# Performance work log

Measured on AMD Instinct MI355X. Metric: run time of the kernel, lower is better.

Reference implementation:

```python
import jax, jax.numpy as jnp
import numpy as np

B, S, D_IN, D_MODEL = 128, 2048, 512, 2048
M, NSY, H, T = 25, 64, 8, 10
REP = NSY * (NSY + 1) // 2
OUT_DIMS = S * 2
DH = D_IN // H
IU, JU = np.triu_indices(NSY)
IDX_OUT = np.arange(NSY)                      # 'first-last': first n neurons for out sync
IDX_ACT = np.arange(D_MODEL - NSY, D_MODEL)   # last n neurons for action sync


def _ln(x, g, b):
    mu = x.mean(-1, keepdims=True)
    var = x.var(-1, keepdims=True)
    return (x - mu) / jnp.sqrt(var + 1e-5) * g + b


def _sync(act, alpha, beta, r, idx):
    # pairwise upper-triangle outer product without materializing (B,n,n)
    sel = act[:, idx]
    pair = sel[:, IU] * sel[:, JU]  # (B, REP)
    if alpha is None:
        alpha, beta = pair, jnp.ones_like(pair)
    else:
        alpha = r * alpha + pair
        beta = r * beta + 1.0
    return alpha / jnp.sqrt(beta), alpha, beta


def _forward(tokens, emb, W_pos, b_pos, Wq, bq, Wk, bk, Wv, bv, Wo, bo, Ws, bs,
             ln_s_g, ln_s_b, ln_n_g, ln_n_b, Wn, bn, temp, Wout, bout,
             start_act, start_trace, decay_action, decay_out):
    # rotary-style learned positional embedding: rotate [0,1] by theta in [0,180deg]
    thetas = jnp.deg2rad(jnp.linspace(0.0, 180.0, S))
    rotated = jnp.stack([-jnp.sin(thetas), jnp.cos(thetas)], -1)  # (S,2)
    pe = rotated @ W_pos + b_pos                                   # (S, D_IN)
    feats = emb[tokens] + pe[None]                                 # (B,S,D_IN)
    kh = (feats @ Wk + bk).reshape(B, S, H, DH)
    vh = (feats @ Wv + bv).reshape(B, S, H, DH)
    r_a = jnp.exp(-decay_action)[None]
    r_o = jnp.exp(-decay_out)[None]
    act = jnp.broadcast_to(start_act[None], (B, D_MODEL))
    trace = jnp.broadcast_to(start_trace[None], (B, D_MODEL, M))
    a_a = b_a = a_o = b_o = None
    preds, certs = [], []
    for _ in range(T):
        s_act, a_a, b_a = _sync(act, a_a, b_a, r_a, IDX_ACT)
        q = (s_act @ Wq + bq).reshape(B, H, DH)
        scores = jnp.einsum('bhd,bshd->bhs', q, kh) / np.float32(np.sqrt(DH))
        attn = jax.nn.softmax(scores, -1)
        o = jnp.einsum('bhs,bshd->bhd', attn, vh).reshape(B, D_IN) @ Wo + bo
        # SynapseNet: Linear -> GLU -> LayerNorm
        pre = jnp.concatenate([o, act], -1) @ Ws + bs
        g1, g2 = jnp.split(pre, 2, -1)
        state = _ln(g1 * jax.nn.sigmoid(g2), ln_s_g, ln_s_b)  # (B, D_MODEL)
        trace = jnp.concatenate([trace[:, :, 1:], state[:, :, None]], -1)
        # NLM: per-neuron linear over memory, GLU, temperature
        xn = _ln(trace, ln_n_g, ln_n_b)
        y = jnp.einsum('bnm,mon->bno', xn, Wn) + bn  # (B, D_MODEL, 2)
        act = (y[..., 0] * jax.nn.sigmoid(y[..., 1])) / temp
        s_out, a_o, b_o = _sync(act, a_o, b_o, r_o, IDX_OUT)
        pred = s_out @ Wout + bout  # (B, OUT_DIMS)
        preds.append(pred)
        logits = pred.reshape(B, S, 2)
        p = jax.nn.softmax(logits, -1)
        ent = -(p * jax.nn.log_softmax(logits, -1)).sum(-1) / np.float32(np.log(2.0))
        ne = ent.mean(-1)
        certs.append(jnp.stack([ne, 1.0 - ne], -1))
    return jnp.stack(preds, -1), jnp.stack(certs, -1)  # (B,OUT_DIMS,T),(B,2,T)


def setup_inputs() -> dict:
    key = jax.random.key(0)
    ks = jax.random.split(key, 16)
    def n(k, shape, s=0.02):
        return (jax.random.normal(k, shape) * s).astype(jnp.float32)
    bound = 1.0 / np.sqrt(M + 2)
    return {
        'tokens': jax.random.randint(ks[0], (B, S), 0, 2, dtype=jnp.int32),
        'emb': n(ks[1], (2, D_IN), 1.0),
        'W_pos': n(ks[2], (2, D_IN)), 'b_pos': jnp.zeros((D_IN,)),
        'Wq': n(ks[3], (REP, D_IN)), 'bq': jnp.zeros((D_IN,)),
        'Wk': n(ks[4], (D_IN, D_IN)), 'bk': jnp.zeros((D_IN,)),
        'Wv': n(ks[5], (D_IN, D_IN)), 'bv': jnp.zeros((D_IN,)),
        'Wo': n(ks[6], (D_IN, D_IN)), 'bo': jnp.zeros((D_IN,)),
        'Ws': n(ks[7], (D_IN + D_MODEL, 2 * D_MODEL)), 'bs': jnp.zeros((2 * D_MODEL,)),
        'ln_s_g': jnp.ones((D_MODEL,)), 'ln_s_b': jnp.zeros((D_MODEL,)),
        'ln_n_g': jnp.ones((M,)), 'ln_n_b': jnp.zeros((M,)),
        'Wn': jax.random.uniform(ks[8], (M, 2, D_MODEL), minval=-bound, maxval=bound),
        'bn': jnp.zeros((1, D_MODEL, 2)),
        'temp': jnp.ones((1,)),
        'Wout': n(ks[9], (REP, OUT_DIMS)), 'bout': jnp.zeros((OUT_DIMS,)),
        'start_act': n(ks[10], (D_MODEL,), 1.0),
        'start_trace': n(ks[11], (D_MODEL, M), 1.0),
        'decay_action': jax.random.uniform(ks[12], (REP,), minval=0.0, maxval=1.0),
        'decay_out': jax.random.uniform(ks[13], (REP,), minval=0.0, maxval=1.0),
    }


def reference(tokens, emb, W_pos, b_pos, Wq, bq, Wk, bk, Wv, bv, Wo, bo, Ws, bs,
              ln_s_g, ln_s_b, ln_n_g, ln_n_b, Wn, bn, temp, Wout, bout,
              start_act, start_trace, decay_action, decay_out):
    return _forward(tokens, emb, W_pos, b_pos, Wq, bq, Wk, bk, Wv, bv, Wo, bo, Ws, bs,
                    ln_s_g, ln_s_b, ln_n_g, ln_n_b, Wn, bn, temp, Wout, bout,
                    start_act, start_trace, decay_action, decay_out)
```

## Files before the change

### kernel.cpp

```cpp
#include <hip/hip_runtime.h>
#include <hip/hip_bf16.h>
#include <math.h>

#define B_ 128
#define S_ 2048
#define D_IN_ 512
#define D_MODEL_ 2048
#define M_ 25
#define NSY_ 64
#define H_ 8
#define T_ 10
#define REP_ 2080
#define DH_ 64
#define PRED_N (B_ * 4096)

typedef unsigned short ushort_t;
typedef __bf16 bf16x8 __attribute__((ext_vector_type(8)));
typedef float f32x4 __attribute__((ext_vector_type(4)));
typedef unsigned short us8 __attribute__((ext_vector_type(8)));

__device__ __forceinline__ ushort_t f2bf(float f) {
    __hip_bfloat16 h = __float2bfloat16(f);
    return *(ushort_t*)&h;
}
// ... 90 lines not shown
    const ushort_t* __restrict__ A, int lda,
    const ushort_t* __restrict__ Bt, int ldb,
    const float* __restrict__ bias,
    float* __restrict__ C, int ldc,
    int M, int N, int K, int kchunk)
{
    const int nb = blockIdx.x, mb = blockIdx.y, zb = blockIdx.z;
    const int k0 = zb * kchunk;
    const int k1 = min(K, k0 + kchunk);
    __shared__ ushort_t As[64][40];
    __shared__ ushort_t Bs[128][40];

    const int tid  = threadIdx.x;
    const int wave = tid >> 6;
    const int lane = tid & 63;
    const int quad = lane >> 4;
    const int mrow = lane & 15;

    f32x4 acc[4][2];
    #pragma unroll
    for (int s = 0; s < 4; s++)
        #pragma unroll
        for (int u = 0; u < 2; u++)
            acc[s][u] = (f32x4){0.f, 0.f, 0.f, 0.f};

    const int arow = tid >> 2, akc = (tid & 3) * 8;
    const int brow = tid >> 1, bkc = (tid & 1) * 16;

    for (int kk0 = k0; kk0 < k1; kk0 += 32) {
        {
            const ushort_t* ap = A + (size_t)(mb * 64 + arow) * lda + kk0 + akc;
            *(us8*)&As[arow][akc] = *(const us8*)ap;
        }
        {
            const ushort_t* bp = Bt + (size_t)(nb * 128 + brow) * ldb + kk0 + bkc;
            *(us8*)&Bs[brow][bkc]     = *(const us8*)bp;
            *(us8*)&Bs[brow][bkc + 8] = *(const us8*)(bp + 8);
        }
        __syncthreads();

        bf16x8 af[4], bfr[2];
        #pragma unroll
        for (int s = 0; s < 4; s++)
            af[s] = *(const bf16x8*)&As[s * 16 + mrow][quad * 8];
        #pragma unroll
        for (int u = 0; u < 2; u++)
            bfr[u] = *(const bf16x8*)&Bs[wave * 32 + u * 16 + mrow][quad * 8];
        #pragma unroll
        for (int s = 0; s < 4; s++)
            #pragma unroll
            for (int u = 0; u < 2; u++)
                acc[s][u] = __builtin_amdgcn_mfma_f32_16x16x32_bf16(
                    af[s], bfr[u], acc[s][u], 0, 0, 0);
        __syncthreads();
    }

    if (gridDim.z == 1) {
        #pragma unroll
        for (int s = 0; s < 4; s++)
            #pragma unroll
            for (int u = 0; u < 2; u++) {
                const int col = nb * 128 + wave * 32 + u * 16 + mrow;
                #pragma unroll
                for (int reg = 0; reg < 4; reg++) {
                    const int row = mb * 64 + s * 16 + quad * 4 + reg;
                    C[(size_t)row * ldc + col] = acc[s][u][reg] + bias[col];
                }
            }
    } else {
        #pragma unroll
        for (int s = 0; s < 4; s++)
            #pragma unroll
            for (int u = 0; u < 2; u++) {
                const int col = nb * 128 + wave * 32 + u * 16 + mrow;
                #pragma unroll
                for (int reg = 0; reg < 4; reg++) {
                    const int row = mb * 64 + s * 16 + quad * 4 + reg;
                    atomicAdd(&C[(size_t)row * ldc + col], acc[s][u][reg]);
                }
            }
    }
}

__global__ __launch_bounds__(256) void gemm_bb_dual(
    const ushort_t* __restrict__ A1, int lda1,
    const ushort_t* __restrict__ Bt1, int ldb1,
    float* __restrict__ C1, int ldc1, int kc1, int nb1x, int nblk1,
    const ushort_t* __restrict__ A2, int lda2,
    const ushort_t* __restrict__ Bt2, int ldb2,
    float* __restrict__ C2, int ldc2, int kc2, int nb2x)
{
    int bid = blockIdx.x;
    const ushort_t* A; const ushort_t* Bt; float* C;
    int lda, ldb, ldc, nb, mb, zb, kchunk;
    if (bid < nblk1) {
        A = A1; Bt = Bt1; C = C1; lda = lda1; ldb = ldb1; ldc = ldc1; kchunk = kc1;
        nb = bid % nb1x; mb = (bid / nb1x) & 1; zb = bid / (nb1x * 2);
    } else {
        bid -= nblk1;
        A = A2; Bt = Bt2; C = C2; lda = lda2; ldb = ldb2; ldc = ldc2; kchunk = kc2;
        nb = bid % nb2x; mb = (bid / nb2x) & 1; zb = bid / (nb2x * 2);
    }
    const int k0 = zb * kchunk;
    const int k1 = min(REP_, k0 + kchunk);
    __shared__ ushort_t As[64][40];
    __shared__ ushort_t Bs[128][40];

    const int tid  = threadIdx.x;
    const int wave = tid >> 6;
    const int lane = tid & 63;
    const int quad = lane >> 4;
    const int mrow = lane & 15;

    f32x4 acc[4][2];
    #pragma unroll
    for (int s = 0; s < 4; s++)
        #pragma unroll
        for (int u = 0; u < 2; u++)
            acc[s][u] = (f32x4){0.f, 0.f, 0.f, 0.f};

    const int arow = tid >> 2, akc = (tid & 3) * 8;
    const int brow = tid >> 1, bkc = (tid & 1) * 16;

    for (int kk0 = k0; kk0 < k1; kk0 += 32) {
        {
            const ushort_t* ap = A + (size_t)(mb * 64 + arow) * lda + kk0 + akc;
            *(us8*)&As[arow][akc] = *(const us8*)ap;
        }
        {
            const ushort_t* bp = Bt + (size_t)(nb * 128 + brow) * ldb + kk0 + bkc;
            *(us8*)&Bs[brow][bkc]     = *(const us8*)bp;
            *(us8*)&Bs[brow][bkc + 8] = *(const us8*)(bp + 8);
        }
        __syncthreads();

        bf16x8 af[4], bfr[2];
        #pragma unroll
        for (int s = 0; s < 4; s++)
            af[s] = *(const bf16x8*)&As[s * 16 + mrow][quad * 8];
        #pragma unroll
        for (int u = 0; u < 2; u++)
            bfr[u] = *(const bf16x8*)&Bs[wave * 32 + u * 16 + mrow][quad * 8];
        #pragma unroll
        for (int s = 0; s < 4; s++)
            #pragma unroll
            for (int u = 0; u < 2; u++)
                acc[s][u] = __builtin_amdgcn_mfma_f32_16x16x32_bf16(
                    af[s], bfr[u], acc[s][u], 0, 0, 0);
        __syncthreads();
    }

    #pragma unroll
    for (int s = 0; s < 4; s++)
        #pragma unroll
        for (int u = 0; u < 2; u++) {
            const int col = nb * 128 + wave * 32 + u * 16 + mrow;
            #pragma unroll
            for (int reg = 0; reg < 4; reg++) {
                const int row = mb * 64 + s * 16 + quad * 4 + reg;
                atomicAdd(&C[(size_t)row * ldc + col], acc[s][u][reg]);
            }
        }
}

__global__ __launch_bounds__(256) void gemm_qk(
    const float* __restrict__ q,
    const ushort_t* __restrict__ Kb,
    float* __restrict__ sc)
{
    const int nb = blockIdx.x, mb = blockIdx.y, z = blockIdx.z;
    const int c = z >> 3, h = z & 7;
    __shared__ ushort_t As[64][40];
    __shared__ ushort_t Bs[128][40];

    const int tid  = threadIdx.x;
    const int wave = tid >> 6;
    const int lane = tid & 63;
    const int quad = lane >> 4;
    const int mrow = lane & 15;

    f32x4 acc[4][2];
    #pragma unroll
    for (int s = 0; s < 4; s++)
        #pragma unroll
        for (int u = 0; u < 2; u++)
            acc[s][u] = (f32x4){0.f, 0.f, 0.f, 0.f};

    const int arow = tid >> 2, akc = (tid & 3) * 8;
    const int brow = tid >> 1, bkc = (tid & 1) * 16;
    const float* Abase = q + (size_t)h * 64;
    const ushort_t* Bbase = Kb + (size_t)c * S_ * 512 + h * 64;

    #pragma unroll
    for (int kk0 = 0; kk0 < 64; kk0 += 32) {
        {
            const float* ap = Abase + (size_t)(mb * 64 + arow) * 512 + kk0 + akc;
            float4 v0 = *(const float4*)ap;
            float4 v1 = *(const float4*)(ap + 4);
            us8 w = { f2bf(v0.x), f2bf(v0.y), f2bf(v0.z), f2bf(v0.w),
                      f2bf(v1.x), f2bf(v1.y), f2bf(v1.z), f2bf(v1.w) };
            *(us8*)&As[arow][akc] = w;
        }
        {
            const ushort_t* bp = Bbase + (size_t)(nb * 128 + brow) * 512 + kk0 + bkc;
            *(us8*)&Bs[brow][bkc]     = *(const us8*)bp;
            *(us8*)&Bs[brow][bkc + 8] = *(const us8*)(bp + 8);
        }
        __syncthreads();

        bf16x8 af[4], bfr[2];
        #pragma unroll
        for (int s = 0; s < 4; s++)
            af[s] = *(const bf16x8*)&As[s * 16 + mrow][quad * 8];
        #pragma unroll
        for (int u = 0; u < 2; u++)
            bfr[u] = *(const bf16x8*)&Bs[wave * 32 + u * 16 + mrow][quad * 8];
        #pragma unroll
        for (int s = 0; s < 4; s++)
            #pragma unroll
            for (int u = 0; u < 2; u++)
                acc[s][u] = __builtin_amdgcn_mfma_f32_16x16x32_bf16(
                    af[s], bfr[u], acc[s][u], 0, 0, 0);
        __syncthreads();
    }

    float* Cb = sc + (size_t)z * 128 * S_;
    #pragma unroll
    for (int s = 0; s < 4; s++)
        #pragma unroll
        for (int u = 0; u < 2; u++) {
            const int col = nb * 128 + wave * 32 + u * 16 + mrow;
            #pragma unroll
            for (int reg = 0; reg < 4; reg++) {
                const int row = mb * 64 + s * 16 + quad * 4 + reg;
                Cb[(size_t)row * S_ + col] = 0.125f * acc[s][u][reg];
            }
        }
}

__global__ __launch_bounds__(256) void attn_soft(
    const float* __restrict__ sc,
    const int*   __restrict__ tokens,
    ushort_t* __restrict__ P,
    float* __restrict__ o,
    float* __restrict__ cat,
    const float* __restrict__ bo,
    const float* __restrict__ bs,
    float* __restrict__ pre)
{
    const int bh = blockIdx.x;
    const int b = bh >> 3, h = bh & 7;
    __shared__ float red[256];
    const int tid = threadIdx.x;

    if (bh < 256) {
        const int idx = bh * 256 + tid;
        cat[(size_t)(idx >> 9) * 2560 + (idx & 511)] = bo[idx & 511];
    } else if (bh < 320) {
        const int idx = (bh - 256) * 256 + tid;
        *(float4*)&o[idx * 4] = make_float4(0.f, 0.f, 0.f, 0.f);
    } else if (bh < 832) {
        const int idx = (bh - 320) * 256 + tid;
        const float4* bs4 = (const float4*)bs;
        ((float4*)pre)[idx] = bs4[idx & 1023];
    }

    const float* sc0 = sc + ((size_t)h * 128 + b) * S_;
    const float* sc1 = sc + ((size_t)(8 + h) * 128 + b) * S_;
    const int* trow = tokens + (size_t)b * S_;

    int tok[8]; float sel[8];
    float lmax = -1e30f;
    #pragma unroll
    for (int i = 0; i < 8; i++) {
        const int s = tid + i * 256;
        tok[i] = trow[s];
        sel[i] = tok[i] ? sc1[s] : sc0[s];
        lmax = fmaxf(lmax, sel[i]);
    }
    red[tid] = lmax; __syncthreads();
    for (int off = 128; off > 0; off >>= 1) {
        if (tid < off) red[tid] = fmaxf(red[tid], red[tid + off]);
        __syncthreads();
    }
    const float mx = red[0];
    __syncthreads();

    float e[8];
    float lsum = 0.f;
    #pragma unroll
    for (int i = 0; i < 8; i++) {
        e[i] = expf(sel[i] - mx);
        lsum += e[i];
    }
    red[tid] = lsum; __syncthreads();
    for (int off = 128; off > 0; off >>= 1) {
        if (tid < off) red[tid] += red[tid + off];
        __syncthreads();
    }
    const float inv = 1.f / red[0];

    ushort_t* Pb = P + ((size_t)h * 128 + b) * 4096;
    #pragma unroll
    for (int i = 0; i < 8; i++) {
        const int s = tid + i * 256;
        const unsigned p = (unsigned)f2bf(e[i] * inv);
        const unsigned word = tok[i] ? (p << 16) : p;
        *(unsigned*)&Pb[s * 2] = word;
    }
}

__global__ __launch_bounds__(256) void gemm_pv(
    const ushort_t* __restrict__ P,
    const ushort_t* __restrict__ VT,
    float* __restrict__ o)
{
    const int mb = blockIdx.x, h = blockIdx.y, zb = blockIdx.z;
    const int k0 = zb * 512;
    __shared__ ushort_t As[64][40];
    __shared__ ushort_t Bs[64][40];

    const int tid  = threadIdx.x;
    const int wave = tid >> 6;
    const int lane = tid & 63;
    const int quad = lane >> 4;
    const int mrow = lane & 15;

    f32x4 acc[4];
    #pragma unroll
    for (int s = 0; s < 4; s++) acc[s] = (f32x4){0.f, 0.f, 0.f, 0.f};

    const int row = tid >> 2, kc = (tid & 3) * 8;
    const ushort_t* Ab = P  + ((size_t)h * 128 + mb * 64 + row) * 4096;
    const ushort_t* Bb = VT + ((size_t)h * 64 + row) * 4096;

    for (int kk = k0; kk < k0 + 512; kk += 32) {
        *(us8*)&As[row][kc] = *(const us8*)(Ab + kk + kc);
        *(us8*)&Bs[row][kc] = *(const us8*)(Bb + kk + kc);
        __syncthreads();
        bf16x8 bfr = *(const bf16x8*)&Bs[wave * 16 + mrow][quad * 8];
        #pragma unroll
        for (int s = 0; s < 4; s++) {
            bf16x8 af = *(const bf16x8*)&As[s * 16 + mrow][quad * 8];
            acc[s] = __builtin_amdgcn_mfma_f32_16x16x32_bf16(af, bfr, acc[s], 0, 0, 0);
        }
        __syncthreads();
    }

    const int col = h * 64 + wave * 16 + mrow;
    #pragma unroll
    for (int s = 0; s < 4; s++)
        #pragma unroll
        for (int reg = 0; reg < 4; reg++) {
            const int rowi = mb * 64 + s * 16 + quad * 4 + reg;
            atomicAdd(&o[(size_t)rowi * 512 + col], acc[s][reg]);
        }
}

__global__ void build_vt(const float* __restrict__ Vtab, ushort_t* __restrict__ VT)
{
    const int gid = blockIdx.x * 256 + threadIdx.x;
    const int k = gid & 4095;
    const int d = (gid >> 12) & 63;
    const int h = gid >> 18;
    const int s = k >> 1, c = k & 1;
    VT[gid] = f2bf(Vtab[((size_t)(c * S_ + s)) * 512 + h * 64 + d]);
}

__global__ void build_sync_tabs(const float* __restrict__ dec_act,
                                const float* __restrict__ dec_out,
                                int* __restrict__ ijtab,
                                float* __restrict__ r_act,
                                float* __restrict__ r_out,
                                float* __restrict__ sqb_act,
                                float* __restrict__ sqb_out)
{
    const int p = blockIdx.x * 256 + threadIdx.x;
    if (p >= REP_) return;
    int i = 0, rem = p;
    while (rem >= NSY_ - i) { rem -= NSY_ - i; i++; }
    ijtab[p] = (i << 16) | (i + rem);
    const float ra = expf(-dec_act[p]);
    const float ro = expf(-dec_out[p]);
    r_act[p] = ra; r_out[p] = ro;
    float ba = 1.f, bo2 = 1.f;
    sqb_act[p] = 1.f;
    sqb_out[p] = 1.f;
    for (int t = 1; t < T_; t++) {
        ba  = ra * ba  + 1.f;
        bo2 = ro * bo2 + 1.f;
        sqb_act[(size_t)t * REP_ + p] = sqrtf(ba);
        sqb_out[(size_t)t * REP_ + p] = sqrtf(bo2);
    }
}

__global__ __launch_bounds__(256) void transpose_bf16_kernel(
    const float* __restrict__ in, ushort_t* __restrict__ out, int K, int N)
{
    __shared__ float tile[32][33];
    const int k0 = blockIdx.y * 32, n0 = blockIdx.x * 32;
    const int tx = threadIdx.x & 31, ty4 = (threadIdx.x >> 5) * 4;
    #pragma unroll
    for (int i = 0; i < 4; i++)
        tile[ty4 + i][tx] = in[(size_t)(k0 + ty4 + i) * N + n0 + tx];
    __syncthreads();
    #pragma unroll
    for (int i = 0; i < 4; i++)
        out[(size_t)(n0 + ty4 + i) * K + k0 + tx] = f2bf(tile[tx][ty4 + i]);
}

__global__ void cast_bf16_kernel(const float* __restrict__ src,
                                 __hip_bfloat16* __restrict__ dst, int n)
{
    const int gid = (blockIdx.x * 256 + threadIdx.x) * 4;
    if (gid >= n) return;
    float4 v = *(const float4*)(src + gid);
    dst[gid + 0] = __float2bfloat16(v.x);
    dst[gid + 1] = __float2bfloat16(v.y);
    dst[gid + 2] = __float2bfloat16(v.z);
    dst[gid + 3] = __float2bfloat16(v.w);
}

__global__ void feats_kernel(const float* __restrict__ emb,
                             const float* __restrict__ Wp,
                             const float* __restrict__ bp,
                             float* __restrict__ f2)
{
    const int gid = blockIdx.x * 256 + threadIdx.x;
    const int k = gid & 511;
    const int s = (gid >> 9) & (S_ - 1);
    const int c = gid >> 20;
    const float th = 3.14159265358979323846f * (float)s / (float)(S_ - 1);
    f2[gid] = emb[c * 512 + k] + (-sinf(th)) * Wp[k] + cosf(th) * Wp[512 + k] + bp[k];
}

__global__ void init_act_kernel(const float* __restrict__ sa,
                                float* __restrict__ act,
                                float* __restrict__ cat)
{
    const int gid = blockIdx.x * 256 + threadIdx.x;
    const int b = gid >> 11, n = gid & 2047;
    const float v = sa[n];
    act[gid] = v;
    cat[(size_t)b * 2560 + 512 + n] = v;
}

__global__ void init_trace_kernel(const float* __restrict__ st,
                                  float* __restrict__ trace)
{
    const int gid = blockIdx.x * 256 + threadIdx.x;
    trace[gid] = st[gid % (D_MODEL_ * M_)];
}

__global__ void sync_kernel(const float* __restrict__ act,
                            float* __restrict__ alpha,
                            const float* __restrict__ decay,
                            const int t, const int off,
                            ushort_t* __restrict__ sout,
                            float* __restrict__ ib1, const float* __restrict__ bias1, int iN1,
                            float* __restrict__ ib2, const float* __restrict__ bias2, int iN2)
{
    const int b = blockIdx.x;
    const int tid = threadIdx.x;
    if (blockIdx.y == 8) {
        if (ib1)
            for (int n = tid; n < iN1; n += 256)
                ib1[(size_t)b * iN1 + n] = bias1[n];
        if (ib2)
            for (int n = tid; n < iN2; n += 256)
                ib2[(size_t)b * iN2 + n] = bias2[n];
    }
    const int p = blockIdx.y * 256 + tid;
    if (p >= REP_) return;
    int i = 0, rem = p;
    while (rem >= NSY_ - i) { rem -= NSY_ - i; i++; }
    const int j = i + rem;
    const float si = act[(size_t)b * D_MODEL_ + off + i];
    const float sj = act[(size_t)b * D_MODEL_ + off + j];
    const float pair = si * sj;
    const float r = expf(-decay[p]);
    float a;
    if (t == 0) a = pair;
    else        a = r * alpha[(size_t)b * REP_ + p] + pair;
    alpha[(size_t)b * REP_ + p] = a;
    float bta = 1.f;
    for (int k = 0; k < t; k++) bta = r * bta + 1.f;
    sout[(size_t)b * REP_ + p] = f2bf(a / sqrtf(bta));
}

__global__ __launch_bounds__(512, 2) void state_trace_kernel(
    const float* __restrict__ pre,
    const float* __restrict__ g,
    const float* __restrict__ bt,
    float* __restrict__ trace,
    const float* __restrict__ ln_g,
    const float* __restrict__ ln_b,
    const float* __restrict__ Wn,
    const float* __restrict__ bn,
    const float* __restrict__ temp,
    float* __restrict__ act,
    float* __restrict__ cat,
    const int t,
    const int* __restrict__ ijtab,
    const float* __restrict__ r_out,
    const float* __restrict__ sqb_out,
    float* __restrict__ a_o,
    ushort_t* __restrict__ s_outb,
    const float* __restrict__ bout,
    float* __restrict__ predt,
    const float* __restrict__ r_act,
    const float* __restrict__ sqb_act,
    float* __restrict__ a_a,
    ushort_t* __restrict__ s_actb,
    const float* __restrict__ bq,
    float* __restrict__ qbuf,
    const int do_act)
{
    const int b = blockIdx.x >> 1, half = blockIdx.x & 1;
    const int tid = threadIdx.x;
    __shared__ float v[D_MODEL_];
    __shared__ float r1[512], r2[512];
    __shared__ float sh_sync[64];
    float s1 = 0.f, s2 = 0.f;
    #pragma unroll
    for (int i = 0; i < 4; i++) {
        const int dd = tid + i * 512;
        const float g1 = pre[(size_t)b * 4096 + dd];
        const float g2 = pre[(size_t)b * 4096 + 2048 + dd];
        const float val = g1 * (1.f / (1.f + expf(-g2)));
        v[dd] = val; s1 += val; s2 += val * val;
    }
    r1[tid] = s1; r2[tid] = s2; __syncthreads();
    for (int off = 256; off > 0; off >>= 1) {
        if (tid < off) { r1[tid] += r1[tid + off]; r2[tid] += r2[tid + off]; }
        __syncthreads();
    }
    const float mu = r1[0] * (1.f / D_MODEL_);
    const float var = fmaxf(r2[0] * (1.f / D_MODEL_) - mu * mu, 0.f);
    const float sinv = 1.f / sqrtf(var + 1e-5f);
    const float tval = temp[0];

    #pragma unroll
    for (int i = 0; i < 2; i++) {
        const int n = half * 1024 + i * 512 + tid;
        const float sval = (v[n] - mu) * sinv * g[n] + bt[n];
        const int gid = b * 2048 + n;
        float* tr = trace + (size_t)gid * M_;
        float x[M_];
        #pragma unroll
        for (int m = 0; m < M_ - 1; m++) x[m] = tr[m + 1];
        x[M_ - 1] = sval;
        #pragma unroll
        for (int m = 0; m < M_; m++) tr[m] = x[m];
        float t1 = 0.f, t2 = 0.f;
        #pragma unroll
        for (int m = 0; m < M_; m++) { t1 += x[m]; t2 += x[m] * x[m]; }
        const float tmu = t1 * (1.f / M_);
        const float tvar = fmaxf(t2 * (1.f / M_) - tmu * tmu, 0.f);
        const float tinv = 1.f / sqrtf(tvar + 1e-5f);
        float y0 = bn[n * 2 + 0], y1 = bn[n * 2 + 1];
        #pragma unroll
        for (int m = 0; m < M_; m++) {
            const float xn = (x[m] - tmu) * tinv * ln_g[m] + ln_b[m];
            y0 += xn * Wn[(size_t)(m * 2 + 0) * D_MODEL_ + n];
            y1 += xn * Wn[(size_t)(m * 2 + 1) * D_MODEL_ + n];
        }
        const float a = y0 * (1.f / (1.f + expf(-y1))) / tval;
        act[gid] = a;
        cat[(size_t)b * 2560 + 512 + n] = a;
        if (half == 0) {
            if (i == 0 && tid < 64) sh_sync[tid] = a;
        } else {
            if (i == 1 && tid >= 448) sh_sync[tid - 448] = a;
        }
    }
    __syncthreads();

    if (half == 0) {
        for (int p = tid; p < REP_; p += 512) {
            const int ij = ijtab[p];
            const float pair = sh_sync[ij >> 16] * sh_sync[ij & 0xffff];
            const float r = r_out[p];
            float a2;
            if (t == 0) a2 = pair;
            else        a2 = r * a_o[(size_t)b * REP_ + p] + pair;
            a_o[(size_t)b * REP_ + p] = a2;
            s_outb[(size_t)b * REP_ + p] = f2bf(a2 / sqb_out[(size_t)t * REP_ + p]);
        }
        const float4* b4 = (const float4*)bout;
        float4* pd = (float4*)(predt + (size_t)b * 4096);
        for (int idx = tid; idx < 1024; idx += 512) pd[idx] = b4[idx];
    } else if (do_act) {
        for (int p = tid; p < REP_; p += 512) {
            const int ij = ijtab[p];
            const float pair = sh_sync[ij >> 16] * sh_sync[ij & 0xffff];
            const float r = r_act[p];
            float a2 = r * a_a[(size_t)b * REP_ + p] + pair;
            a_a[(size_t)b * REP_ + p] = a2;
            s_actb[(size_t)b * REP_ + p] = f2bf(a2 / sqb_act[(size_t)(t + 1) * REP_ + p]);
        }
        const float4* b4 = (const float4*)bq;
        float4* qb = (float4*)(qbuf + (size_t)b * 512);
        if (tid < 128) qb[tid] = b4[tid];
    }
}

__global__ __launch_bounds__(256) void ent_all_kernel(
    const float* __restrict__ predst,
    float* __restrict__ certbf)
{
    const int t = blockIdx.x >> 7;
    const int b = blockIdx.x & 127;
    const int tid = threadIdx.x;
    __shared__ float red[256];
    const float* pr = predst + (size_t)t * PRED_N + (size_t)b * 4096;
    float sum = 0.f;
    #pragma unroll
    for (int i = 0; i < 8; i++) {
        const int s = tid + i * 256;
        const float l0 = pr[2 * s], l1 = pr[2 * s + 1];
        const float mm = fmaxf(l0, l1);
        const float z0 = expf(l0 - mm), z1 = expf(l1 - mm);
        const float Z = z0 + z1;
        const float lz = logf(Z);
        const float p0 = z0 / Z, p1 = z1 / Z;
        const float lp0 = (l0 - mm) - lz, lp1 = (l1 - mm) - lz;
        sum += -(p0 * lp0 + p1 * lp1) * 1.4426950408889634f;
    }
    red[tid] = sum; __syncthreads();
    for (int off = 128; off > 0; off >>= 1) {
        if (tid < off) red[tid] += red[tid + off];
        __syncthreads();
    }
    if (tid == 0) {
        const float ne = red[0] * (1.f / S_);
        certbf[(size_t)t * B_ * 2 + b * 2 + 0] = ne;
        certbf[(size_t)t * B_ * 2 + b * 2 + 1] = 1.f - ne;
    }
}

__global__ __launch_bounds__(256) void finalize_kernel(
    const float* __restrict__ predstage,
    const float* __restrict__ certbuf,
    float* __restrict__ dout)
{
    __shared__ float tile[T_][1024];
    const int tid = threadIdx.x;
    const int row0 = blockIdx.x * 1024;
    #pragma unroll
    for (int t = 0; t < T_; t++) {
        float4 v = *(const float4*)(predstage + (size_t)t * PRED_N + row0 + tid * 4);
        tile[t][tid * 4 + 0] = v.x; tile[t][tid * 4 + 1] = v.y;
        tile[t][tid * 4 + 2] = v.z; tile[t][tid * 4 + 3] = v.w;
    }
    __syncthreads();
    float buf[40];
    #pragma unroll
    for (int r = 0; r < 4; r++)
        #pragma unroll
        for (int t = 0; t < T_; t++)
            buf[r * 10 + t] = tile[t][tid * 4 + r];
    float* dst = dout + (size_t)(row0 + tid * 4) * T_;
    #pragma unroll
    for (int k = 0; k < 10; k++)
        *(float4*)(dst + k * 4) = make_float4(buf[4*k], buf[4*k+1], buf[4*k+2], buf[4*k+3]);

    if (blockIdx.x == 0 && tid < B_) {
        const int b = tid;
        const size_t base = (size_t)PRED_N * T_;
        #pragma unroll
        for (int t = 0; t < T_; t++) {
            dout[base + (size_t)(b * 2 + 0) * T_ + t] = certbuf[t * B_ * 2 + b * 2 + 0];
            dout[base + (size_t)(b * 2 + 1) * T_ + t] = certbuf[t * B_ * 2 + b * 2 + 1];
        }
    }
}

extern "C" void kernel_launch(void* const* d_in, const int* in_sizes, int n_in,
                              void* d_out, int out_size, void* d_ws, size_t ws_size,
                              hipStream_t stream)
{
    const int*   tokens    = (const int*)  d_in[0];
    const float* emb       = (const float*)d_in[1];
    const float* W_pos     = (const float*)d_in[2];
    const float* b_pos     = (const float*)d_in[3];
    const float* Wq        = (const float*)d_in[4];
    const float* bq        = (const float*)d_in[5];
    const float* Wk        = (const float*)d_in[6];
    const float* bk        = (const float*)d_in[7];
    const float* Wv        = (const float*)d_in[8];
    const float* bv        = (const float*)d_in[9];
    const float* Wo        = (const float*)d_in[10];
    const float* bo        = (const float*)d_in[11];
    const float* Ws        = (const float*)d_in[12];
    const float* bs        = (const float*)d_in[13];
    const float* ln_s_g    = (const float*)d_in[14];
    const float* ln_s_b    = (const float*)d_in[15];
    const float* ln_n_g    = (const float*)d_in[16];
    const float* ln_n_b    = (const float*)d_in[17];
    const float* Wn        = (const float*)d_in[18];
    const float* bn        = (const float*)d_in[19];
    const float* temp      = (const float*)d_in[20];
    const float* Wout      = (const float*)d_in[21];
    const float* bout      = (const float*)d_in[22];
    const float* start_act = (const float*)d_in[23];
    const float* start_tr  = (const float*)d_in[24];
    const float* dec_act   = (const float*)d_in[25];
    const float* dec_out   = (const float*)d_in[26];
    float* out = (float*)d_out;
    float* w = (float*)d_ws;

    size_t off = 0;
    float* f2     = w + off; off += (size_t)2 * S_ * 512;
    float* Ktab   = w + off; off += (size_t)2 * S_ * 512;
    float* Vtab   = w + off; off += (size_t)2 * S_ * 512;
    float* act    = w + off; off += (size_t)B_ * D_MODEL_;
    float* cat    = w + off; off += (size_t)B_ * 2560;
    float* a_a    = w + off; off += (size_t)B_ * REP_;
    float* a_o    = w + off; off += (size_t)B_ * REP_;
    float* qbuf   = w + off; off += (size_t)B_ * 512;
    float* o_attn = w + off; off += (size_t)B_ * 512;
    float* pre    = w + off; off += (size_t)B_ * 4096;
    float* trace  = w + off; off += (size_t)B_ * D_MODEL_ * M_;
    float* scbuf  = w + off; off += (size_t)16 * 128 * S_;
    float* predst = w + off; off += (size_t)T_ * PRED_N;
    float* certbf = w + off; off += (size_t)T_ * B_ * 2;
    ushort_t* s_actb = (ushort_t*)(w + off); off += (size_t)B_ * REP_ / 2;
    ushort_t* s_outb = (ushort_t*)(w + off); off += (size_t)B_ * REP_ / 2;
    __hip_bfloat16* Kb = (__hip_bfloat16*)(w + off); off += (size_t)S_ * 512;
    ushort_t* Pbuf  = (ushort_t*)(w + off); off += (size_t)8 * 128 * 4096 / 2;
    ushort_t* VT    = (ushort_t*)(w + off); off += (size_t)8 * 64 * 4096 / 2;
    ushort_t* WkT   = (ushort_t*)(w + off); off += (size_t)512 * 512 / 2;
    ushort_t* WvT   = (ushort_t*)(w + off); off += (size_t)512 * 512 / 2;
    ushort_t* WqT   = (ushort_t*)(w + off); off += (size_t)512 * REP_ / 2;
    ushort_t* WoT   = (ushort_t*)(w + off); off += (size_t)512 * 512 / 2;
    ushort_t* WsT   = (ushort_t*)(w + off); off += (size_t)4096 * 2560 / 2;
    ushort_t* WoutT = (ushort_t*)(w + off); off += (size_t)4096 * REP_ / 2;
    int*   ijtab = (int*)(w + off); off += REP_;
    float* r_actT = w + off; off += REP_;
    float* r_outT = w + off; off += REP_;
    float* sqb_a  = w + off; off += (size_t)T_ * REP_;
    float* sqb_o  = w + off; off += (size_t)T_ * REP_;

    feats_kernel<<<(2 * S_ * 512) / 256, 256, 0, stream>>>(emb, W_pos, b_pos, f2);
    init_act_kernel<<<(B_ * D_MODEL_) / 256, 256, 0, stream>>>(start_act, act, cat);
    init_trace_kernel<<<(B_ * D_MODEL_ * M_) / 256, 256, 0, stream>>>(start_tr, trace);
    build_sync_tabs<<<(REP_ + 255) / 256, 256, 0, stream>>>(
        dec_act, dec_out, ijtab, r_actT, r_outT, sqb_a, sqb_o);

    transpose_bf16_kernel<<<dim3(512 / 32, 512 / 32), 256, 0, stream>>>(Wk, WkT, 512, 512);
    transpose_bf16_kernel<<<dim3(512 / 32, 512 / 32), 256, 0, stream>>>(Wv, WvT, 512, 512);
    transpose_bf16_kernel<<<dim3(512 / 32, REP_ / 32), 256, 0, stream>>>(Wq, WqT, REP_, 512);
    transpose_bf16_kernel<<<dim3(512 / 32, 512 / 32), 256, 0, stream>>>(Wo, WoT, 512, 512);
    transpose_bf16_kernel<<<dim3(4096 / 32, 2560 / 32), 256, 0, stream>>>(Ws, WsT, 2560, 4096);
    transpose_bf16_kernel<<<dim3(4096 / 32, REP_ / 32), 256, 0, stream>>>(Wout, WoutT, REP_, 4096);

    gemm_bf16<<<dim3(512 / 128, (2 * S_) / 64, 1), 256, 0, stream>>>(
        f2, 512, WkT, 512, bk, Ktab, 512, 2 * S_, 512, 512, 512);
    gemm_bf16<<<dim3(512 / 128, (2 * S_) / 64, 1), 256, 0, stream>>>(
        f2, 512, WvT, 512, bv, Vtab, 512, 2 * S_, 512, 512, 512);
    cast_bf16_kernel<<<(2 * S_ * 512 / 4) / 256, 256, 0, stream>>>(Ktab, Kb, 2 * S_ * 512);
    build_vt<<<(8 * 64 * 4096) / 256, 256, 0, stream>>>(Vtab, VT);

    sync_kernel<<<dim3(B_, 9), 256, 0, stream>>>(
        act, a_a, dec_act, 0, D_MODEL_ - NSY_, s_actb,
        qbuf, bq, 512, nullptr, nullptr, 0);
    gemm_bb<<<dim3(512 / 128, 2, 13), 256, 0, stream>>>(
        s_actb, REP_, WqT, REP_, bq, qbuf, 512, B_, 512, REP_, 160);

    for (int t = 0; t < T_; t++) {
        gemm_qk<<<dim3(S_ / 128, 2, 16), 256, 0, stream>>>(
            qbuf, (const ushort_t*)Kb, scbuf);
        attn_soft<<<B_ * H_, 256, 0, stream>>>(
            scbuf, tokens, Pbuf, o_attn, cat, bo, bs, pre);
        gemm_pv<<<dim3(2, 8, 8), 256, 0, stream>>>(Pbuf, VT, o_attn);

        gemm_bf16<<<dim3(512 / 128, 2, 8), 256, 0, stream>>>(
            o_attn, 512, WoT, 512, bo, cat, 2560, B_, 512, 512, 64);

        gemm_bf16<<<dim3(4096 / 128, 2, 8), 256, 0, stream>>>(
            cat, 2560, WsT, 2560, bs, pre, 4096, B_, 4096, 2560, 320);

        float* predt = predst + (size_t)t * PRED_N;
        state_trace_kernel<<<B_ * 2, 512, 0, stream>>>(
            pre, ln_s_g, ln_s_b, trace, ln_n_g, ln_n_b, Wn, bn, temp, act, cat,
            t, ijtab,
            r_outT, sqb_o, a_o, s_outb, bout, predt,
            r_actT, sqb_a, a_a, s_actb, bq, qbuf, (t < T_ - 1) ? 1 : 0);

        const int blocks2 = (t < T_ - 1) ? 104 : 0;
        gemm_bb_dual<<<dim3(320 + blocks2), 256, 0, stream>>>(
            s_outb, REP_, WoutT, REP_, predt, 4096, 416, 32, 320,
            s_actb, REP_, WqT, REP_, qbuf, 512, 160, 4);
    }

    ent_all_kernel<<<T_ * B_, 256, 0, stream>>>(predst, certbf);
    finalize_kernel<<<PRED_N / 1024, 256, 0, stream>>>(predst, certbf, out);
}
```

Measured before the change: 1.216 ms.

## Fold Wo into Ws, split the synapse GEMM, and turn the trace into a ring buffer

Precomputes a combined Wo·Ws weight and bias so the attention output goes straight into the synapse pre-activation, removing the per-step Wo GEMM and the concat buffer. The activation half of the synapse GEMM for the next step is computed inside a merged triple kernel, together with the out-sync and action-sync GEMMs, using double-buffered pre arrays. The trace update becomes a ring buffer indexed by a compile-time step, writing one slot instead of shifting all 25. Init and transpose kernels are also merged into single launches. In exchange it adds a one-time weight-combination GEMM and changes the rounding path, since the Wo·Ws product is rounded to bf16.

```diff
diff --git a/kernel.cpp b/kernel.cpp
--- a/kernel.cpp
+++ b/kernel.cpp
@@ -196,31 +196,12 @@
     }
 }
 
-__global__ __launch_bounds__(256) void gemm_bb_dual(
-    const ushort_t* __restrict__ A1, int lda1,
-    const ushort_t* __restrict__ Bt1, int ldb1,
-    float* __restrict__ C1, int ldc1, int kc1, int nb1x, int nblk1,
-    const ushort_t* __restrict__ A2, int lda2,
-    const ushort_t* __restrict__ Bt2, int ldb2,
-    float* __restrict__ C2, int ldc2, int kc2, int nb2x)
-{
-    int bid = blockIdx.x;
-    const ushort_t* A; const ushort_t* Bt; float* C;
-    int lda, ldb, ldc, nb, mb, zb, kchunk;
-    if (bid < nblk1) {
-        A = A1; Bt = Bt1; C = C1; lda = lda1; ldb = ldb1; ldc = ldc1; kchunk = kc1;
-        nb = bid % nb1x; mb = (bid / nb1x) & 1; zb = bid / (nb1x * 2);
-    } else {
-        bid -= nblk1;
-        A = A2; Bt = Bt2; C = C2; lda = lda2; ldb = ldb2; ldc = ldc2; kchunk = kc2;
-        nb = bid % nb2x; mb = (bid / nb2x) & 1; zb = bid / (nb2x * 2);
-    }
-    const int k0 = zb * kchunk;
-    const int k1 = min(REP_, k0 + kchunk);
-    __shared__ ushort_t As[64][40];
-    __shared__ ushort_t Bs[128][40];
-
-    const int tid  = threadIdx.x;
+__device__ __forceinline__ void g_tile128(
+    const ushort_t* Ap, int lda, const ushort_t* Bt, int ldb,
+    float* C, int ldc, int nb, int mb, int k0, int k1, char* smem, int tid)
+{
+    ushort_t (*As)[40] = (ushort_t(*)[40])smem;
+    ushort_t (*Bs)[40] = (ushort_t(*)[40])(smem + 64 * 40 * 2);
     const int wave = tid >> 6;
     const int lane = tid & 63;
     const int quad = lane >> 4;
@@ -238,7 +219,7 @@
 
     for (int kk0 = k0; kk0 < k1; kk0 += 32) {
         {
-            const ushort_t* ap = A + (size_t)(mb * 64 + arow) * lda + kk0 + akc;
+            const ushort_t* ap = Ap + (size_t)(mb * 64 + arow) * lda + kk0 + akc;
             *(us8*)&As[arow][akc] = *(const us8*)ap;
         }
         {
@@ -275,6 +256,36 @@
                 atomicAdd(&C[(size_t)row * ldc + col], acc[s][u][reg]);
             }
         }
+}
+
+__global__ __launch_bounds__(256) void triple_kernel(
+    const ushort_t* __restrict__ s_outb, const ushort_t* __restrict__ WoutT,
+    float* __restrict__ predt,
+    const ushort_t* __restrict__ s_actb, const ushort_t* __restrict__ WqT,
+    float* __restrict__ qbuf,
+    const ushort_t* __restrict__ actb, const ushort_t* __restrict__ WsT,
+    float* __restrict__ pre_nxt)
+{
+    __shared__ __align__(16) char smem[15360];
+    const int vb = blockIdx.x, tid = threadIdx.x;
+    if (vb < 320) {
+        const int nb = vb & 31, mb = (vb >> 5) & 1, zb = vb >> 6;
+        const int k0 = zb * 416;
+        g_tile128(s_outb, REP_, WoutT, REP_, predt, 4096,
+                  nb, mb, k0, min(REP_, k0 + 416), smem, tid);
+    } else if (vb < 424) {
+        const int v2 = vb - 320;
+        const int nb = v2 & 3, mb = (v2 >> 2) & 1, zb = v2 >> 3;
+        const int k0 = zb * 160;
+        g_tile128(s_actb, REP_, WqT, REP_, qbuf, 512,
+                  nb, mb, k0, min(REP_, k0 + 160), smem, tid);
+    } else {
+        const int v3 = vb - 424;
+        const int nb = v3 & 31, mb = (v3 >> 5) & 1, zb = v3 >> 6;
+        const int k0 = zb * 256;
+        g_tile128(actb, 2048, WsT + 512, 2560, pre_nxt, 4096,
+                  nb, mb, k0, k0 + 256, smem, tid);
+    }
 }
 
 __global__ __launch_bounds__(256) void gemm_qk(
@@ -357,26 +368,21 @@
     const int*   __restrict__ tokens,
     ushort_t* __restrict__ P,
     float* __restrict__ o,
-    float* __restrict__ cat,
-    const float* __restrict__ bo,
-    const float* __restrict__ bs,
-    float* __restrict__ pre)
+    const float* __restrict__ bs2,
+    float* __restrict__ pre_nxt)
 {
     const int bh = blockIdx.x;
     const int b = bh >> 3, h = bh & 7;
     __shared__ float red[256];
     const int tid = threadIdx.x;
 
-    if (bh < 256) {
+    if (bh < 512) {
         const int idx = bh * 256 + tid;
-        cat[(size_t)(idx >> 9) * 2560 + (idx & 511)] = bo[idx & 511];
-    } else if (bh < 320) {
-        const int idx = (bh - 256) * 256 + tid;
-        *(float4*)&o[idx * 4] = make_float4(0.f, 0.f, 0.f, 0.f);
-    } else if (bh < 832) {
-        const int idx = (bh - 320) * 256 + tid;
-        const float4* bs4 = (const float4*)bs;
-        ((float4*)pre)[idx] = bs4[idx & 1023];
+        const float4* bs4 = (const float4*)bs2;
+        ((float4*)pre_nxt)[idx] = bs4[idx & 1023];
+    } else if (bh < 576) {
+        const int idx = (bh - 512) * 256 + tid;
+        ((float4*)o)[idx] = make_float4(0.f, 0.f, 0.f, 0.f);
     }
 
     const float* sc0 = sc + ((size_t)h * 128 + b) * S_;
@@ -481,38 +487,83 @@
     VT[gid] = f2bf(Vtab[((size_t)(c * S_ + s)) * 512 + h * 64 + d]);
 }
 
-__global__ void build_sync_tabs(const float* __restrict__ dec_act,
-                                const float* __restrict__ dec_out,
-                                int* __restrict__ ijtab,
-                                float* __restrict__ r_act,
-                                float* __restrict__ r_out,
-                                float* __restrict__ sqb_act,
-                                float* __restrict__ sqb_out)
-{
-    const int p = blockIdx.x * 256 + threadIdx.x;
-    if (p >= REP_) return;
-    int i = 0, rem = p;
-    while (rem >= NSY_ - i) { rem -= NSY_ - i; i++; }
-    ijtab[p] = (i << 16) | (i + rem);
-    const float ra = expf(-dec_act[p]);
-    const float ro = expf(-dec_out[p]);
-    r_act[p] = ra; r_out[p] = ro;
-    float ba = 1.f, bo2 = 1.f;
-    sqb_act[p] = 1.f;
-    sqb_out[p] = 1.f;
-    for (int t = 1; t < T_; t++) {
-        ba  = ra * ba  + 1.f;
-        bo2 = ro * bo2 + 1.f;
-        sqb_act[(size_t)t * REP_ + p] = sqrtf(ba);
-        sqb_out[(size_t)t * REP_ + p] = sqrtf(bo2);
-    }
-}
-
-__global__ __launch_bounds__(256) void transpose_bf16_kernel(
-    const float* __restrict__ in, ushort_t* __restrict__ out, int K, int N)
-{
+#define IA_FE 8192
+#define IA_AC (IA_FE + 1024)
+#define IA_TR (IA_AC + 6400)
+#define IA_SY (IA_TR + 9)
+#define IA_NB (IA_SY + 1)
+__global__ void init_all(const float* __restrict__ emb, const float* __restrict__ Wp,
+                         const float* __restrict__ bp, float* __restrict__ f2,
+                         const float* __restrict__ sa, float* __restrict__ act,
+                         ushort_t* __restrict__ actb,
+                         const float* __restrict__ st, float* __restrict__ trace,
+                         const float* __restrict__ dec_act, const float* __restrict__ dec_out,
+                         int* __restrict__ ijtab, float* __restrict__ r_act,
+                         float* __restrict__ r_out, float* __restrict__ sqb_a,
+                         float* __restrict__ sqb_o, float* __restrict__ zerov)
+{
+    const int vb = blockIdx.x, tid = threadIdx.x;
+    if (vb < IA_FE) {
+        const int gid = vb * 256 + tid;
+        const int k = gid & 511;
+        const int s = (gid >> 9) & (S_ - 1);
+        const int c = gid >> 20;
+        const float th = 3.14159265358979323846f * (float)s / (float)(S_ - 1);
+        f2[gid] = emb[c * 512 + k] + (-sinf(th)) * Wp[k] + cosf(th) * Wp[512 + k] + bp[k];
+    } else if (vb < IA_AC) {
+        const int gid = (vb - IA_FE) * 256 + tid;
+        const int n = gid & 2047;
+        const float v = sa[n];
+        act[gid] = v;
+        actb[gid] = f2bf(v);
+    } else if (vb < IA_TR) {
+        const int idx4 = (vb - IA_AC) * 256 + tid;
+        ((float4*)trace)[idx4] = ((const float4*)st)[idx4 % 12800];
+    } else if (vb < IA_SY) {
+        const int p = (vb - IA_TR) * 256 + tid;
+        if (p >= REP_) return;
+        int i = 0, rem = p;
+        while (rem >= NSY_ - i) { rem -= NSY_ - i; i++; }
+        ijtab[p] = (i << 16) | (i + rem);
+        const float ra = expf(-dec_act[p]);
+        const float ro = expf(-dec_out[p]);
+        r_act[p] = ra; r_out[p] = ro;
+        float ba = 1.f, bo2 = 1.f;
+        sqb_a[p] = 1.f;
+        sqb_o[p] = 1.f;
+        for (int t = 1; t < T_; t++) {
+            ba  = ra * ba  + 1.f;
+            bo2 = ro * bo2 + 1.f;
+            sqb_a[(size_t)t * REP_ + p] = sqrtf(ba);
+            sqb_o[(size_t)t * REP_ + p] = sqrtf(bo2);
+        }
+    } else {
+        #pragma unroll
+        for (int k = 0; k < 4; k++)
+            ((float4*)zerov)[tid * 4 + k] = make_float4(0.f, 0.f, 0.f, 0.f);
+    }
+}
+
+__global__ __launch_bounds__(256) void transpose_all(
+    const float* __restrict__ Wk, ushort_t* __restrict__ WkT,
+    const float* __restrict__ Wv, ushort_t* __restrict__ WvT,
+    const float* __restrict__ Wq, ushort_t* __restrict__ WqT,
+    const float* __restrict__ Wo, ushort_t* __restrict__ WoT,
+    const float* __restrict__ Ws, ushort_t* __restrict__ WsT,
+    const float* __restrict__ Wout, ushort_t* __restrict__ WoutT)
+{
+    int bid = blockIdx.x;
+    const float* in; ushort_t* out; int K, N;
+    if      (bid <   256) {              in = Wk;   out = WkT;   K = 512;  N = 512;  }
+    else if (bid <   512) { bid -=  256; in = Wv;   out = WvT;   K = 512;  N = 512;  }
+    else if (bid <  1552) { bid -=  512; in = Wq;   out = WqT;   K = 2080; N = 512;  }
+    else if (bid <  1808) { bid -= 1552; in = Wo;   out = WoT;   K = 512;  N = 512;  }
+    else if (bid < 12048) { bid -= 1808; in = Ws;   out = WsT;   K = 2560; N = 4096; }
+    else                  { bid -= 12048; in = Wout; out = WoutT; K = 2080; N = 4096; }
+    const int bxw = N >> 5;
+    const int bx = bid % bxw, by = bid / bxw;
     __shared__ float tile[32][33];
-    const int k0 = blockIdx.y * 32, n0 = blockIdx.x * 32;
+    const int k0 = by * 32, n0 = bx * 32;
     const int tx = threadIdx.x & 31, ty4 = (threadIdx.x >> 5) * 4;
     #pragma unroll
     for (int i = 0; i < 4; i++)
@@ -535,35 +586,14 @@
     dst[gid + 3] = __float2bfloat16(v.w);
 }
 
-__global__ void feats_kernel(const float* __restrict__ emb,
-                             const float* __restrict__ Wp,
-                             const float* __restrict__ bp,
-                             float* __restrict__ f2)
-{
-    const int gid = blockIdx.x * 256 + threadIdx.x;
-    const int k = gid & 511;
-    const int s = (gid >> 9) & (S_ - 1);
-    const int c = gid >> 20;
-    const float th = 3.14159265358979323846f * (float)s / (float)(S_ - 1);
-    f2[gid] = emb[c * 512 + k] + (-sinf(th)) * Wp[k] + cosf(th) * Wp[512 + k] + bp[k];
-}
-
-__global__ void init_act_kernel(const float* __restrict__ sa,
-                                float* __restrict__ act,
-                                float* __restrict__ cat)
-{
-    const int gid = blockIdx.x * 256 + threadIdx.x;
-    const int b = gid >> 11, n = gid & 2047;
-    const float v = sa[n];
-    act[gid] = v;
-    cat[(size_t)b * 2560 + 512 + n] = v;
-}
-
-__global__ void init_trace_kernel(const float* __restrict__ st,
-                                  float* __restrict__ trace)
-{
-    const int gid = blockIdx.x * 256 + threadIdx.x;
-    trace[gid] = st[gid % (D_MODEL_ * M_)];
+__global__ void bs2_kernel(const float* __restrict__ bs, const float* __restrict__ bo,
+                           const float* __restrict__ Ws, float* __restrict__ bs2)
+{
+    const int n = blockIdx.x * 256 + threadIdx.x;
+    float acc = bs[n];
+    for (int j = 0; j < 512; j++)
+        acc += bo[j] * Ws[(size_t)j * 4096 + n];
+    bs2[n] = acc;
 }
 
 __global__ void sync_kernel(const float* __restrict__ act,
@@ -602,7 +632,8 @@
     sout[(size_t)b * REP_ + p] = f2bf(a / sqrtf(bta));
 }
 
-__global__ __launch_bounds__(512, 2) void state_trace_kernel(
+template<int TT>
+__global__ __launch_bounds__(512, 2) void st_kernel(
     const float* __restrict__ pre,
     const float* __restrict__ g,
     const float* __restrict__ bt,
@@ -612,9 +643,7 @@
     const float* __restrict__ Wn,
     const float* __restrict__ bn,
     const float* __restrict__ temp,
-    float* __restrict__ act,
-    float* __restrict__ cat,
-    const int t,
+    ushort_t* __restrict__ actb,
     const int* __restrict__ ijtab,
     const float* __restrict__ r_out,
     const float* __restrict__ sqb_out,
@@ -627,8 +656,7 @@
     float* __restrict__ a_a,
     ushort_t* __restrict__ s_actb,
     const float* __restrict__ bq,
-    float* __restrict__ qbuf,
-    const int do_act)
+    float* __restrict__ qbuf)
 {
     const int b = blockIdx.x >> 1, half = blockIdx.x & 1;
     const int tid = threadIdx.x;
@@ -662,10 +690,13 @@
         float* tr = trace + (size_t)gid * M_;
         float x[M_];
         #pragma unroll
-        for (int m = 0; m < M_ - 1; m++) x[m] = tr[m + 1];
+        for (int m = 0; m < M_ - 1; m++) {
+            int slot = TT + 1 + m;
+            if (slot >= M_) slot -= M_;
+            x[m] = tr[slot];
+        }
         x[M_ - 1] = sval;
-        #pragma unroll
-        for (int m = 0; m < M_; m++) tr[m] = x[m];
+        tr[TT] = sval;
         float t1 = 0.f, t2 = 0.f;
         #pragma unroll
         for (int m = 0; m < M_; m++) { t1 += x[m]; t2 += x[m] * x[m]; }
@@ -680,8 +711,7 @@
             y1 += xn * Wn[(size_t)(m * 2 + 1) * D_MODEL_ + n];
         }
         const float a = y0 * (1.f / (1.f + expf(-y1))) / tval;
-        act[gid] = a;
-        cat[(size_t)b * 2560 + 512 + n] = a;
+        actb[gid] = f2bf(a);
         if (half == 0) {
             if (i == 0 && tid < 64) sh_sync[tid] = a;
         } else {
@@ -696,22 +726,22 @@
             const float pair = sh_sync[ij >> 16] * sh_sync[ij & 0xffff];
             const float r = r_out[p];
             float a2;
-            if (t == 0) a2 = pair;
-            else        a2 = r * a_o[(size_t)b * REP_ + p] + pair;
+            if (TT == 0) a2 = pair;
+            else         a2 = r * a_o[(size_t)b * REP_ + p] + pair;
             a_o[(size_t)b * REP_ + p] = a2;
-            s_outb[(size_t)b * REP_ + p] = f2bf(a2 / sqb_out[(size_t)t * REP_ + p]);
+            s_outb[(size_t)b * REP_ + p] = f2bf(a2 / sqb_out[(size_t)TT * REP_ + p]);
         }
         const float4* b4 = (const float4*)bout;
         float4* pd = (float4*)(predt + (size_t)b * 4096);
         for (int idx = tid; idx < 1024; idx += 512) pd[idx] = b4[idx];
-    } else if (do_act) {
+    } else if (TT < T_ - 1) {
         for (int p = tid; p < REP_; p += 512) {
             const int ij = ijtab[p];
             const float pair = sh_sync[ij >> 16] * sh_sync[ij & 0xffff];
             const float r = r_act[p];
             float a2 = r * a_a[(size_t)b * REP_ + p] + pair;
             a_a[(size_t)b * REP_ + p] = a2;
-            s_actb[(size_t)b * REP_ + p] = f2bf(a2 / sqb_act[(size_t)(t + 1) * REP_ + p]);
+            s_actb[(size_t)b * REP_ + p] = f2bf(a2 / sqb_act[(size_t)(TT + 1) * REP_ + p]);
         }
         const float4* b4 = (const float4*)bq;
         float4* qb = (float4*)(qbuf + (size_t)b * 512);
@@ -829,18 +859,22 @@
     float* Ktab   = w + off; off += (size_t)2 * S_ * 512;
     float* Vtab   = w + off; off += (size_t)2 * S_ * 512;
     float* act    = w + off; off += (size_t)B_ * D_MODEL_;
-    float* cat    = w + off; off += (size_t)B_ * 2560;
     float* a_a    = w + off; off += (size_t)B_ * REP_;
     float* a_o    = w + off; off += (size_t)B_ * REP_;
     float* qbuf   = w + off; off += (size_t)B_ * 512;
     float* o_attn = w + off; off += (size_t)B_ * 512;
-    float* pre    = w + off; off += (size_t)B_ * 4096;
+    float* pre0   = w + off; off += (size_t)B_ * 4096;
+    float* pre1   = w + off; off += (size_t)B_ * 4096;
     float* trace  = w + off; off += (size_t)B_ * D_MODEL_ * M_;
     float* scbuf  = w + off; off += (size_t)16 * 128 * S_;
     float* predst = w + off; off += (size_t)T_ * PRED_N;
     float* certbf = w + off; off += (size_t)T_ * B_ * 2;
+    float* Wcomb32= w + off; off += (size_t)4096 * 512;
+    float* bs2    = w + off; off += 4096;
+    float* zerov  = w + off; off += 4096;
     ushort_t* s_actb = (ushort_t*)(w + off); off += (size_t)B_ * REP_ / 2;
     ushort_t* s_outb = (ushort_t*)(w + off); off += (size_t)B_ * REP_ / 2;
+    ushort_t* actb   = (ushort_t*)(w + off); off += (size_t)B_ * D_MODEL_ / 2;
     __hip_bfloat16* Kb = (__hip_bfloat16*)(w + off); off += (size_t)S_ * 512;
     ushort_t* Pbuf  = (ushort_t*)(w + off); off += (size_t)8 * 128 * 4096 / 2;
     ushort_t* VT    = (ushort_t*)(w + off); off += (size_t)8 * 64 * 4096 / 2;
@@ -850,62 +884,77 @@
     ushort_t* WoT   = (ushort_t*)(w + off); off += (size_t)512 * 512 / 2;
     ushort_t* WsT   = (ushort_t*)(w + off); off += (size_t)4096 * 2560 / 2;
     ushort_t* WoutT = (ushort_t*)(w + off); off += (size_t)4096 * REP_ / 2;
-    int*   ijtab = (int*)(w + off); off += REP_;
+    ushort_t* WoC   = (ushort_t*)(w + off); off += (size_t)512 * 512 / 2;
+    ushort_t* WcombTb=(ushort_t*)(w + off); off += (size_t)4096 * 512 / 2;
+    int*   ijtab  = (int*)(w + off); off += REP_;
     float* r_actT = w + off; off += REP_;
     float* r_outT = w + off; off += REP_;
     float* sqb_a  = w + off; off += (size_t)T_ * REP_;
     float* sqb_o  = w + off; off += (size_t)T_ * REP_;
 
-    feats_kernel<<<(2 * S_ * 512) / 256, 256, 0, stream>>>(emb, W_pos, b_pos, f2);
-    init_act_kernel<<<(B_ * D_MODEL_) / 256, 256, 0, stream>>>(start_act, act, cat);
-    init_trace_kernel<<<(B_ * D_MODEL_ * M_) / 256, 256, 0, stream>>>(start_tr, trace);
-    build_sync_tabs<<<(REP_ + 255) / 256, 256, 0, stream>>>(
-        dec_act, dec_out, ijtab, r_actT, r_outT, sqb_a, sqb_o);
-
-    transpose_bf16_kernel<<<dim3(512 / 32, 512 / 32), 256, 0, stream>>>(Wk, WkT, 512, 512);
-    transpose_bf16_kernel<<<dim3(512 / 32, 512 / 32), 256, 0, stream>>>(Wv, WvT, 512, 512);
-    transpose_bf16_kernel<<<dim3(512 / 32, REP_ / 32), 256, 0, stream>>>(Wq, WqT, REP_, 512);
-    transpose_bf16_kernel<<<dim3(512 / 32, 512 / 32), 256, 0, stream>>>(Wo, WoT, 512, 512);
-    transpose_bf16_kernel<<<dim3(4096 / 32, 2560 / 32), 256, 0, stream>>>(Ws, WsT, 2560, 4096);
-    transpose_bf16_kernel<<<dim3(4096 / 32, REP_ / 32), 256, 0, stream>>>(Wout, WoutT, REP_, 4096);
-
-    gemm_bf16<<<dim3(512 / 128, (2 * S_) / 64, 1), 256, 0, stream>>>(
+    init_all<<<IA_NB, 256, 0, stream>>>(
+        emb, W_pos, b_pos, f2, start_act, act, actb, start_tr, trace,
+        dec_act, dec_out, ijtab, r_actT, r_outT, sqb_a, sqb_o, zerov);
+    transpose_all<<<20368, 256, 0, stream>>>(
+        Wk, WkT, Wv, WvT, Wq, WqT, Wo, WoT, Ws, WsT, Wout, WoutT);
+    gemm_bf16<<<dim3(4, 64, 1), 256, 0, stream>>>(
         f2, 512, WkT, 512, bk, Ktab, 512, 2 * S_, 512, 512, 512);
-    gemm_bf16<<<dim3(512 / 128, (2 * S_) / 64, 1), 256, 0, stream>>>(
+    gemm_bf16<<<dim3(4, 64, 1), 256, 0, stream>>>(
         f2, 512, WvT, 512, bv, Vtab, 512, 2 * S_, 512, 512, 512);
     cast_bf16_kernel<<<(2 * S_ * 512 / 4) / 256, 256, 0, stream>>>(Ktab, Kb, 2 * S_ * 512);
     build_vt<<<(8 * 64 * 4096) / 256, 256, 0, stream>>>(Vtab, VT);
 
+    cast_bf16_kernel<<<(512 * 512 / 4) / 256, 256, 0, stream>>>(
+        Wo, (__hip_bfloat16*)WoC, 512 * 512);
+    gemm_bb<<<dim3(4, 64, 1), 256, 0, stream>>>(
+        WsT, 2560, WoC, 512, zerov, Wcomb32, 512, 4096, 512, 512, 512);
+    cast_bf16_kernel<<<(4096 * 512 / 4) / 256, 256, 0, stream>>>(
+        Wcomb32, (__hip_bfloat16*)WcombTb, 4096 * 512);
+    bs2_kernel<<<16, 256, 0, stream>>>(bs, bo, Ws, bs2);
+
     sync_kernel<<<dim3(B_, 9), 256, 0, stream>>>(
         act, a_a, dec_act, 0, D_MODEL_ - NSY_, s_actb,
-        qbuf, bq, 512, nullptr, nullptr, 0);
-    gemm_bb<<<dim3(512 / 128, 2, 13), 256, 0, stream>>>(
-        s_actb, REP_, WqT, REP_, bq, qbuf, 512, B_, 512, REP_, 160);
+        qbuf, bq, 512, pre0, bs2, 4096);
+    gemm_bb<<<dim3(32, 2, 8), 256, 0, stream>>>(
+        actb, 2048, WsT + 512, 2560, zerov, pre0, 4096, B_, 4096, 2048, 256);
+    gemm_bb<<<dim3(4, 2, 13), 256, 0, stream>>>(
+        s_actb, REP_, WqT, REP_, zerov, qbuf, 512, B_, 512, REP_, 160);
+
+    #define ST_ARGS(PC, PT) \
+        PC, ln_s_g, ln_s_b, trace, ln_n_g, ln_n_b, Wn, bn, temp, actb, \
+        ijtab, r_outT, sqb_o, a_o, s_outb, bout, PT, \
+        r_actT, sqb_a, a_a, s_actb, bq, qbuf
 
     for (int t = 0; t < T_; t++) {
+        float* pre_cur = (t & 1) ? pre1 : pre0;
+        float* pre_nxt = (t & 1) ? pre0 : pre1;
+        float* predt = predst + (size_t)t * PRED_N;
+
         gemm_qk<<<dim3(S_ / 128, 2, 16), 256, 0, stream>>>(
             qbuf, (const ushort_t*)Kb, scbuf);
         attn_soft<<<B_ * H_, 256, 0, stream>>>(
-            scbuf, tokens, Pbuf, o_attn, cat, bo, bs, pre);
+            scbuf, tokens, Pbuf, o_attn, bs2, pre_nxt);
         gemm_pv<<<dim3(2, 8, 8), 256, 0, stream>>>(Pbuf, VT, o_attn);
 
-        gemm_bf16<<<dim3(512 / 128, 2, 8), 256, 0, stream>>>(
-            o_attn, 512, WoT, 512, bo, cat, 2560, B_, 512, 512, 64);
-
-        gemm_bf16<<<dim3(4096 / 128, 2, 8), 256, 0, stream>>>(
-            cat, 2560, WsT, 2560, bs, pre, 4096, B_, 4096, 2560, 320);
-
-        float* predt = predst + (size_t)t * PRED_N;
-        state_trace_kernel<<<B_ * 2, 512, 0, stream>>>(
-            pre, ln_s_g, ln_s_b, trace, ln_n_g, ln_n_b, Wn, bn, temp, act, cat,
-            t, ijtab,
-            r_outT, sqb_o, a_o, s_outb, bout, predt,
-            r_actT, sqb_a, a_a, s_actb, bq, qbuf, (t < T_ - 1) ? 1 : 0);
-
-        const int blocks2 = (t < T_ - 1) ? 104 : 0;
-        gemm_bb_dual<<<dim3(320 + blocks2), 256, 0, stream>>>(
-            s_outb, REP_, WoutT, REP_, predt, 4096, 416, 32, 320,
-            s_actb, REP_, WqT, REP_, qbuf, 512, 160, 4);
+        gemm_bf16<<<dim3(32, 2, 4), 256, 0, stream>>>(
+            o_attn, 512, WcombTb, 512, bs2, pre_cur, 4096, B_, 4096, 512, 128);
+
+        switch (t) {
+            case 0: st_kernel<0><<<B_ * 2, 512, 0, stream>>>(ST_ARGS(pre_cur, predt)); break;
+            case 1: st_kernel<1><<<B_ * 2, 512, 0, stream>>>(ST_ARGS(pre_cur, predt)); break;
+            case 2: st_kernel<2><<<B_ * 2, 512, 0, stream>>>(ST_ARGS(pre_cur, predt)); break;
+            case 3: st_kernel<3><<<B_ * 2, 512, 0, stream>>>(ST_ARGS(pre_cur, predt)); break;
+            case 4: st_kernel<4><<<B_ * 2, 512, 0, stream>>>(ST_ARGS(pre_cur, predt)); break;
+            case 5: st_kernel<5><<<B_ * 2, 512, 0, stream>>>(ST_ARGS(pre_cur, predt)); break;
+            case 6: st_kernel<6><<<B_ * 2, 512, 0, stream>>>(ST_ARGS(pre_cur, predt)); break;
+            case 7: st_kernel<7><<<B_ * 2, 512, 0, stream>>>(ST_ARGS(pre_cur, predt)); break;
+            case 8: st_kernel<8><<<B_ * 2, 512, 0, stream>>>(ST_ARGS(pre_cur, predt)); break;
+            case 9: st_kernel<9><<<B_ * 2, 512, 0, stream>>>(ST_ARGS(pre_cur, predt)); break;
+        }
+
+        const int nblk = (t < T_ - 1) ? 936 : 320;
+        triple_kernel<<<nblk, 256, 0, stream>>>(
+            s_outb, WoutT, predt, s_actb, WqT, qbuf, actb, WsT, pre_nxt);
     }
 
     ent_all_kernel<<<T_ * B_, 256, 0, stream>>>(predst, certbf);
```

After: 1.157 ms. 4.9% less time.
